# Kernel optimization log

Hardware: AMD Instinct MI355X
Metric: run time of the kernel (lower is better)

## Reference

```python
import jax, jax.numpy as jnp
import numpy as np
from jax import lax

DN = ('NCHW', 'OIHW', 'NCHW')

def conv7(x, w, b):
    y = lax.conv_general_dilated(x, w, window_strides=(1, 1), padding='VALID', dimension_numbers=DN)
    return y + b[None, :, None, None]

def maxpool2(x):
    return lax.reduce_window(x, -jnp.inf, lax.max, (1, 1, 2, 2), (1, 1, 2, 2), 'VALID')

def setup_inputs() -> dict:
    key = jax.random.key(0)
    ks = jax.random.split(key, 7)
    B, C, H, W = 8, 64, 70, 70
    x = jax.random.normal(ks[0], (B, C, H, W), dtype=jnp.float32)
    s = 0.05  # small init to keep softmax logits sane
    theta_w = jax.random.normal(ks[1], (100, C, 7, 7), dtype=jnp.float32) * s
    theta_b = jax.random.normal(ks[2], (100,), dtype=jnp.float32) * s
    phi_w = jax.random.normal(ks[3], (100, C, 7, 7), dtype=jnp.float32) * s
    phi_b = jax.random.normal(ks[4], (100,), dtype=jnp.float32) * s
    g_w = jax.random.normal(ks[5], (200, C, 7, 7), dtype=jnp.float32) * s
    g_b = jax.random.normal(ks[6], (200,), dtype=jnp.float32) * s
    return {'x': x, 'theta_w': theta_w, 'theta_b': theta_b, 'phi_w': phi_w, 'phi_b': phi_b, 'g_w': g_w, 'g_b': g_b}

def reference(x, theta_w, theta_b, phi_w, phi_b, g_w, g_b):
    B, C, H, W = x.shape
    h, w = H - 6, W - 6           # VALID 7x7 conv output spatial
    N = h * w                     # 4096
    M = N // 4                    # 1024 (after 2x2 maxpool)
    theta = conv7(x, theta_w, theta_b).reshape(B, 100, N)
    phi = maxpool2(conv7(x, phi_w, phi_b)).reshape(B, 100, M)
    attn = jnp.einsum('bcn,bcm->bnm', theta, phi)                # B x N x M
    attn = jax.nn.softmax(attn, axis=-1)
    g = maxpool2(conv7(x, g_w, g_b)).reshape(B, 200, M)
    attn_g = jnp.einsum('bcm,bnm->bcn', g, attn)
    return attn_g.reshape(B, 200, h, w)
```

## Files before the change

kernel.cpp:

```cpp
#include <hip/hip_runtime.h>
#include <cstdint>
#include <cstddef>

#define BATCH 8
#define CIN 64
#define HIN 70
#define HOUT 64
#define NPIX 4096
#define MPIX 1024

typedef __attribute__((ext_vector_type(8))) short short8;
typedef __attribute__((ext_vector_type(4))) float f32x4;
typedef __attribute__((ext_vector_type(4))) unsigned int uint4v;

__device__ __forceinline__ unsigned short f2bf_rne(float f) {
  unsigned int u = __builtin_bit_cast(unsigned int, f);
  unsigned int r = (u + 0x7FFFu + ((u >> 16) & 1u)) >> 16;
  return (unsigned short)r;
}

__device__ __forceinline__ unsigned int rot16(unsigned int u) {
  return (u >> 16) | (u << 16);
}

__global__ __launch_bounds__(256) void prep_x(const float* __restrict__ x,
                                              unsigned int* __restrict__ xTi,
                                              unsigned int* __restrict__ xTi_h) {
  __shared__ float tile[64][71];
  const int blk = blockIdx.x;
  const int b = blk / 70;
  const int r = blk - b * 70;
  const int t = threadIdx.x;
  for (int i = t; i < 64 * 70; i += 256) {
    int ci = i / 70;
    int c = i - ci * 70;
    tile[ci][c] = x[(((size_t)(b * 64 + ci)) * 70 + r) * 70 + c];
  }
  __syncthreads();
  for (int i = t; i < 70 * 64; i += 256) {
    int c = i >> 6;
    int ci = i & 63;
    float a = tile[ci][c];
    unsigned short hi = f2bf_rne(a);
    float hif = __builtin_bit_cast(float, ((unsigned int)hi) << 16);
    unsigned short lo = f2bf_rne(a - hif);
    xTi[(((size_t)(b * 70 + r)) * 70 + c) * 64 + ci] =
        (unsigned int)hi | (((unsigned int)lo) << 16);
  }
  for (int i = t; i < 70 * 32; i += 256) {
    int c = i >> 5;
    int dwi = i & 31;
    unsigned int h0 = f2bf_rne(tile[2 * dwi][c]);
    unsigned int h1 = f2bf_rne(tile[2 * dwi + 1][c]);
    xTi_h[(((size_t)(b * 70 + r)) * 70 + c) * 32 + dwi] = h0 | (h1 << 16);
  }
}

__global__ __launch_bounds__(256) void prep_w(
    const float* __restrict__ tw, const float* __restrict__ pw,
    const float* __restrict__ gw,
    const float* __restrict__ tb, const float* __restrict__ pb,
    const float* __restrict__ gb,
    unsigned int* __restrict__ wTi, unsigned int* __restrict__ wTi_s,
    float* __restrict__ biasPad) {
  int gid = blockIdx.x * 256 + threadIdx.x;
  if (gid < 1404928) {
    if (gid < 448) {
      float bv = 0.0f;
      if (gid < 100) bv = tb[gid];
      else if (gid < 200) bv = pb[gid - 100];
      else if (gid < 400) bv = gb[gid - 200];
      biasPad[gid] = bv;
    }
    int ci = gid & 63;
    int OC = (gid >> 6) % 448;
    int s = gid / (448 * 64);
    float v = 0.0f;
    if (OC < 100) v = tw[((size_t)(OC * 64 + ci)) * 49 + s];
    else if (OC < 200) v = pw[((size_t)((OC - 100) * 64 + ci)) * 49 + s];
    else if (OC < 400) v = gw[((size_t)((OC - 200) * 64 + ci)) * 49 + s];
    unsigned short hi = f2bf_rne(v);
    float hif = __builtin_bit_cast(float, ((unsigned int)hi) << 16);
    unsigned short lo = f2bf_rne(v - hif);
    wTi[gid] = (unsigned int)hi | (((unsigned int)lo) << 16);
  } else if (gid < 1404928 + 301056) {
    int g2 = gid - 1404928;
    int dwi = g2 & 31;
    int OCl = (g2 >> 5) % 192;
    int s = g2 / (192 * 32);
    int gc = 56 + OCl;
    float v0 = 0.0f, v1 = 0.0f;
    if (gc < 200) {
      v0 = gw[((size_t)(gc * 64 + 2 * dwi)) * 49 + s];
      v1 = gw[((size_t)(gc * 64 + 2 * dwi + 1)) * 49 + s];
    }
    wTi_s[g2] = (unsigned int)f2bf_rne(v0) |
                (((unsigned int)f2bf_rne(v1)) << 16);
  }
}

template <bool DUAL>
__global__ __launch_bounds__(256, 2) void convmfma_kernel(
    const unsigned short* __restrict__ xT,
    const unsigned short* __restrict__ wT,
    const float* __restrict__ biasPad,
    unsigned int* __restrict__ thd_dw,
    unsigned int* __restrict__ phd_dw,
    unsigned short* __restrict__ gP) {
  __shared__ __align__(16) char smem[62720 + 16384];
  const int LDSW = 62720;
  const int NCH = DUAL ? 4 : 2;
  const int XS = DUAL ? 128 : 64;
  const int WOCS = DUAL ? 128 : 64;
  const int WSTRIDE = DUAL ? 57344 : 12288;

  const int gx = blockIdx.x;
  const int b = gx >> 3;
  const int ptile = gx & 7;
  const int oy0 = ptile * 8;
  const int oc0 = (DUAL ? 0 : 256) + (blockIdx.y << 6);
  const int oc0W = DUAL ? oc0 : (blockIdx.y << 6);

  const int t = threadIdx.x;
  const int wv = t >> 6;
  const int l = t & 63;
  const int lm = l & 15;
  const int lg = l >> 4;

  int wdstOff_[2];
  const unsigned short* wsrc_[2];
  const int keyA = ((lm >> 1) & 3) << 4;
  const int laneA = (lm << 6) + ((lg << 4) ^ keyA);

  f32x4 acc[4][2][4];
#pragma unroll
  for (int j = 0; j < 4; ++j)
#pragma unroll
    for (int rr = 0; rr < 2; ++rr)
#pragma unroll
      for (int f = 0; f < 4; ++f) acc[j][rr][f] = (f32x4)0.0f;

  for (int chunk = 0; chunk < NCH; ++chunk) {
    for (int i = t; i < 3920; i += 256) {
      int idx70 = i >> 2;
      int s16 = i & 3;
      int rr = idx70 / 70;
      int cc = idx70 - rr * 70;
      const unsigned short* src =
          xT + ((size_t)((b * 70 + oy0 + rr) * 70 + cc)) * XS +
          (chunk << 5) + (s16 << 3);
      short8 v = *(const short8*)src;
      int dst = (idx70 << 6) + ((s16 << 4) ^ (((cc >> 1) & 3) << 4));
      *(short8*)(smem + dst) = v;
    }
    short8 wreg[2];
#pragma unroll
    for (int u2 = 0; u2 < 2; ++u2) {
      int u = t + (u2 << 8);
      int sub = u >> 8;
      int oc_t = (u >> 2) & 63;
      int q = u & 3;
      wdstOff_[u2] =
          sub * 4096 + (oc_t << 6) + ((q << 4) ^ (((oc_t >> 1) & 3) << 4));
      wsrc_[u2] = wT + (size_t)(oc0W + oc_t) * WOCS + (chunk << 5) + (q << 3);
      wreg[u2] = *(const short8*)(wsrc_[u2] + (size_t)sub * WSTRIDE);
      *(short8*)(smem + LDSW + wdstOff_[u2]) = wreg[u2];
      wreg[u2] = *(const short8*)(wsrc_[u2] + (size_t)(2 + sub) * WSTRIDE);
    }
    __syncthreads();

    for (int p = 0; p < 25; ++p) {
      const char* slotBase = smem + LDSW + ((p & 1) << 13);
#pragma unroll
      for (int halfs = 0; halfs < 2; ++halfs) {
        const int s = 2 * p + halfs;
        if (s <= 48) {
          const int ky = s / 7;
          const int kx = s - ky * 7;
          const char* wb = slotBase + (halfs << 12) + laneA;
          short8 aW[4], aS[4];
#pragma unroll
          for (int j = 0; j < 4; ++j) {
            aW[j] = *(const short8*)(wb + j * 1024);
            if (DUAL) {
              uint4v u = __builtin_bit_cast(uint4v, aW[j]);
              u.x = rot16(u.x); u.y = rot16(u.y);
              u.z = rot16(u.z); u.w = rot16(u.w);
              aS[j] = __builtin_bit_cast(short8, u);
            }
          }
          const int klx = kx + lm;
          const int key = ((klx >> 1) & 3) << 4;
#pragma unroll
          for (int rr = 0; rr < 2; ++rr) {
            const char* bbase =
                smem + ((2 * wv + rr + ky) * 70 + klx) * 64 + ((lg << 4) ^ key);
#pragma unroll
            for (int f = 0; f < 4; ++f) {
              short8 bf = *(const short8*)(bbase + f * 1024);
#pragma unroll
              for (int j = 0; j < 4; ++j) {
                acc[j][rr][f] = __builtin_amdgcn_mfma_f32_16x16x32_bf16(
                    aW[j], bf, acc[j][rr][f], 0, 0, 0);
                if (DUAL)
                  acc[j][rr][f] = __builtin_amdgcn_mfma_f32_16x16x32_bf16(
                      aS[j], bf, acc[j][rr][f], 0, 0, 0);
              }
            }
          }
        }
      }
      if (p < 24) {
#pragma unroll
        for (int u2 = 0; u2 < 2; ++u2) {
          *(short8*)(smem + LDSW + (((p + 1) & 1) << 13) + wdstOff_[u2]) =
              wreg[u2];
          if (p < 23) {
            int sub = (t + (u2 << 8)) >> 8;
            int snext = 2 * (p + 2) + sub;
            if (snext > 48) snext = 48;
            wreg[u2] = *(const short8*)(wsrc_[u2] + (size_t)snext * WSTRIDE);
          }
        }
      }
      __syncthreads();
    }
  }

  float bia[4][4];
#pragma unroll
  for (int j = 0; j < 4; ++j)
#pragma unroll
    for (int r = 0; r < 4; ++r) bia[j][r] = biasPad[oc0 + j * 16 + lg * 4 + r];

  if (DUAL) {
#pragma unroll
    for (int j = 0; j < 4; ++j) {
#pragma unroll
      for (int rr = 0; rr < 2; ++rr) {
#pragma unroll
        for (int f = 0; f < 4; ++f) {
#pragma unroll
          for (int r = 0; r < 4; ++r) {
            int ch = oc0 + j * 16 + lg * 4 + r;
            if (ch < 128) {
              int n = (oy0 + 2 * wv + rr) * 64 + f * 16 + lm;
              unsigned int outw = 0u;
              if (ch < 100) {
                float v = acc[j][rr][f][r] + bia[j][r];
                unsigned short hi = f2bf_rne(v);
                float hif =
                    __builtin_bit_cast(float, ((unsigned int)hi) << 16);
                unsigned short lo = f2bf_rne(v - hif);
                outw = (unsigned int)hi | (((unsigned int)lo) << 16);
              }
              thd_dw[(((size_t)(b << 12) + n) << 7) + ch] = outw;
            }
          }
        }
      }
    }
  }

#pragma unroll
  for (int j = 0; j < 4; ++j) {
#pragma unroll
    for (int f = 0; f < 4; ++f) {
#pragma unroll
      for (int r = 0; r < 4; ++r) {
        float v0 = acc[j][0][f][r] + bia[j][r];
        float v1 = acc[j][1][f][r] + bia[j][r];
        float vr = fmaxf(v0, v1);
        float vn = fmaxf(vr, __shfl_xor(vr, 1));
        if (!(lm & 1)) {
          int ch = oc0 + j * 16 + lg * 4 + r;
          int m = (((oy0 >> 1) + wv) << 5) + f * 8 + (lm >> 1);
          if (DUAL) {
            if (ch >= 100 && ch < 200) {
              int c = ch - 100;
              unsigned short hi = f2bf_rne(vn);
              float hif = __builtin_bit_cast(float, ((unsigned int)hi) << 16);
              unsigned short lo = f2bf_rne(vn - hif);
              phd_dw[(((size_t)(b << 10) + m) << 7) + c] =
                  (unsigned int)hi | (((unsigned int)lo) << 16);
            } else if (ch >= 200) {
              gP[((size_t)(b * 208 + (ch - 200)) << 10) + m] = f2bf_rne(vn);
              if (ch < 228)
                phd_dw[(((size_t)(b << 10) + m) << 7) + (ch - 100)] = 0u;
            }
          } else {
            int cg = ch - 200;
            if (cg < 208)
              gP[((size_t)(b * 208 + cg) << 10) + m] = f2bf_rne(vn);
          }
        }
      }
    }
  }
}

__global__ __launch_bounds__(256) void attn_kernel(
    const unsigned short* __restrict__ thd,
    const unsigned short* __restrict__ phd,
    const unsigned short* __restrict__ gP,
    float* __restrict__ out) {
  __shared__ __align__(16) float outAcc[16][212];
  __shared__ float corrL[16][33];
  __shared__ float statsL[4][16][2];
  __shared__ float mFinL[16];
  __shared__ float invL[16];

  const int bx = blockIdx.x;
  const int b = bx >> 8;
  const int n0 = (bx & 255) << 4;
  const int t = threadIdx.x;
  const int w = t >> 6;
  const int l = t & 63;
  const int lm = l & 15;
  const int lg = l >> 4;

  short8 aA[8], aS[8];
  {
    const unsigned short* ap =
        thd + (((size_t)(b << 12) + n0 + lm) << 8) + lg * 8;
#pragma unroll
    for (int kf = 0; kf < 8; ++kf) {
      short8 v = *(const short8*)(ap + kf * 32);
      aA[kf] = v;
      uint4v u = __builtin_bit_cast(uint4v, v);
      u.x = rot16(u.x); u.y = rot16(u.y); u.z = rot16(u.z); u.w = rot16(u.w);
      aS[kf] = __builtin_bit_cast(short8, u);
    }
  }

  float mRun = -3.0e38f, sRun = 0.0f;
  unsigned int Pr[8][4];

  const int src1 = ((lg & 1) << 5) + lm;
  const int src2 = src1 + 16;
  const bool hi2 = (lg >> 1) != 0;

#pragma unroll
  for (int step = 0; step < 8; ++step) {
    const int m0 = (w << 8) + (step << 5);
    f32x4 ac0 = (f32x4)0.f, ac1 = (f32x4)0.f;
    const unsigned short* bp0 =
        phd + (((size_t)(b << 10) + m0 + lm) << 8) + lg * 8;
    const unsigned short* bp1 = bp0 + (16 << 8);
#pragma unroll
    for (int kf = 0; kf < 8; ++kf) {
      short8 av0 = *(const short8*)(bp0 + kf * 32);
      short8 av1 = *(const short8*)(bp1 + kf * 32);
      ac0 = __builtin_amdgcn_mfma_f32_16x16x32_bf16(av0, aA[kf], ac0, 0, 0, 0);
      ac1 = __builtin_amdgcn_mfma_f32_16x16x32_bf16(av1, aA[kf], ac1, 0, 0, 0);
      ac0 = __builtin_amdgcn_mfma_f32_16x16x32_bf16(av0, aS[kf], ac0, 0, 0, 0);
      ac1 = __builtin_amdgcn_mfma_f32_16x16x32_bf16(av1, aS[kf], ac1, 0, 0, 0);
    }
    float tm = fmaxf(fmaxf(fmaxf(ac0[0], ac0[1]), fmaxf(ac0[2], ac0[3])),
                     fmaxf(fmaxf(ac1[0], ac1[1]), fmaxf(ac1[2], ac1[3])));
    tm = fmaxf(tm, __shfl_xor(tm, 16));
    tm = fmaxf(tm, __shfl_xor(tm, 32));
    float mNew = fmaxf(mRun, tm);
    float scale = __expf(mRun - mNew);
    float p0 = __expf(ac0[0] - mNew), p1 = __expf(ac0[1] - mNew);
    float p2 = __expf(ac0[2] - mNew), p3 = __expf(ac0[3] - mNew);
    float q0 = __expf(ac1[0] - mNew), q1 = __expf(ac1[1] - mNew);
    float q2 = __expf(ac1[2] - mNew), q3 = __expf(ac1[3] - mNew);
    float cs = ((p0 + p1) + (p2 + p3)) + ((q0 + q1) + (q2 + q3));
    cs += __shfl_xor(cs, 16);
    cs += __shfl_xor(cs, 32);
    mRun = mNew;
    sRun = sRun * scale + cs;
    if (l < 16) corrL[lm][(w << 3) + step] = mRun;
    unsigned int d0 = (unsigned int)f2bf_rne(p0) |
                      (((unsigned int)f2bf_rne(p1)) << 16);
    unsigned int d1 = (unsigned int)f2bf_rne(p2) |
                      (((unsigned int)f2bf_rne(p3)) << 16);
    unsigned int e0 = (unsigned int)f2bf_rne(q0) |
                      (((unsigned int)f2bf_rne(q1)) << 16);
    unsigned int e1 = (unsigned int)f2bf_rne(q2) |
                      (((unsigned int)f2bf_rne(q3)) << 16);
    unsigned int A0 = (unsigned int)__shfl((int)d0, src1);
    unsigned int A1 = (unsigned int)__shfl((int)d1, src1);
    unsigned int B0 = (unsigned int)__shfl((int)d0, src2);
    unsigned int B1 = (unsigned int)__shfl((int)d1, src2);
    unsigned int C0 = (unsigned int)__shfl((int)e0, src1);
    unsigned int C1 = (unsigned int)__shfl((int)e1, src1);
    unsigned int D0 = (unsigned int)__shfl((int)e0, src2);
    unsigned int D1 = (unsigned int)__shfl((int)e1, src2);
    Pr[step][0] = hi2 ? C0 : A0;
    Pr[step][1] = hi2 ? C1 : A1;
    Pr[step][2] = hi2 ? D0 : B0;
    Pr[step][3] = hi2 ? D1 : B1;
  }
  if (l < 16) {
    statsL[w][lm][0] = mRun;
    statsL[w][lm][1] = sRun;
  }
  __syncthreads();

  if (t < 16) {
    float mF = -3.0e38f;
#pragma unroll
    for (int qq = 0; qq < 4; ++qq) mF = fmaxf(mF, statsL[qq][t][0]);
    float sF = 0.0f;
#pragma unroll
    for (int qq = 0; qq < 4; ++qq)
      sF += statsL[qq][t][1] * __expf(statsL[qq][t][0] - mF);
    mFinL[t] = mF;
    invL[t] = 1.0f / sF;
  }
  __syncthreads();

  {
    int e = t * 2;
#pragma unroll
    for (int i = 0; i < 2; ++i) {
      int row = (e + i) >> 5;
      int col = (e + i) & 31;
      corrL[row][col] = __expf(corrL[row][col] - mFinL[row]) * invL[row];
    }
  }
  __syncthreads();

#pragma unroll
  for (int s = 0; s < 8; ++s) {
    float corr = corrL[lm][(w << 3) + s];
#pragma unroll
    for (int j = 0; j < 4; ++j) {
      unsigned int u = Pr[s][j];
      float lo = __builtin_bit_cast(float, u << 16);
      float hi = __builtin_bit_cast(float, u & 0xffff0000u);
      Pr[s][j] = (unsigned int)f2bf_rne(lo * corr) |
                 (((unsigned int)f2bf_rne(hi * corr)) << 16);
    }
  }

  f32x4 oacc[13];
#pragma unroll
  for (int i = 0; i < 13; ++i) oacc[i] = (f32x4)0.f;

#pragma unroll
  for (int s = 0; s < 8; ++s) {
    uint4v pu;
    pu.x = Pr[s][0]; pu.y = Pr[s][1]; pu.z = Pr[s][2]; pu.w = Pr[s][3];
    short8 pf = __builtin_bit_cast(short8, pu);
    const unsigned short* gbase =
        gP + ((size_t)(b * 208) << 10) + (w << 8) + (s << 5) + lg * 8;
#pragma unroll
    for (int ct = 0; ct < 13; ++ct) {
      int c = (ct << 4) + lm;
      short8 gv = *(const short8*)(gbase + ((size_t)c << 10));
      oacc[ct] = __builtin_amdgcn_mfma_f32_16x16x32_bf16(pf, gv, oacc[ct], 0, 0, 0);
    }
  }

  for (int rnd = 0; rnd < 4; ++rnd) {
    if (w == rnd) {
#pragma unroll
      for (int ct = 0; ct < 13; ++ct) {
#pragma unroll
        for (int r = 0; r < 4; ++r) {
          int n = (lg << 2) + r;
          int c = (ct << 4) + lm;
          if (rnd == 0) outAcc[n][c] = oacc[ct][r];
          else outAcc[n][c] += oacc[ct][r];
        }
      }
    }
    __syncthreads();
  }

  {
    int lane16 = t & 15;
    int grp = t >> 4;
    for (int c = grp; c < 200; c += 16)
      out[(((size_t)(b * 200 + c)) << 12) + n0 + lane16] = outAcc[lane16][c];
  }
}

extern "C" void kernel_launch(void* const* d_in, const int* in_sizes, int n_in,
                              void* d_out, int out_size, void* d_ws,
                              size_t ws_size, hipStream_t stream) {
  const float* x  = (const float*)d_in[0];
  const float* tw = (const float*)d_in[1];
  const float* tb = (const float*)d_in[2];
  const float* pw = (const float*)d_in[3];
  const float* pb = (const float*)d_in[4];
  const float* gw = (const float*)d_in[5];
  const float* gb = (const float*)d_in[6];
  float* out = (float*)d_out;

  unsigned short* ws_us = (unsigned short*)d_ws;
  unsigned short* thd   = ws_us;
  unsigned short* phd   = ws_us + 8388608;
  unsigned short* gP    = ws_us + 10485760;
  unsigned short* xTi   = ws_us + 12189696;
  unsigned short* wTi   = ws_us + 17207296;
  unsigned short* xTi_h = ws_us + 20017152;
  unsigned short* wTi_s = ws_us + 22525952;
  float* biasPad = (float*)(ws_us + 23128064);

  prep_x<<<560, 256, 0, stream>>>(x, (unsigned int*)xTi, (unsigned int*)xTi_h);
  prep_w<<<6664, 256, 0, stream>>>(tw, pw, gw, tb, pb, gb,
                                   (unsigned int*)wTi, (unsigned int*)wTi_s,
                                   biasPad);

  convmfma_kernel<true><<<dim3(64, 4), 256, 0, stream>>>(
      xTi, wTi, biasPad, (unsigned int*)thd, (unsigned int*)phd, gP);
  convmfma_kernel<false><<<dim3(64, 3), 256, 0, stream>>>(
      xTi_h, wTi_s, biasPad, (unsigned int*)thd, (unsigned int*)phd, gP);
  attn_kernel<<<2048, 256, 0, stream>>>(thd, phd, gP, out);
}
```

Before: 445.1 us.

## Process 32 query rows per attention block to reuse phi and g loads

The attention kernel now handles two 16-row query tiles per block instead of one, halving the grid. Each phi fragment loaded from global memory feeds MFMAs for both query tiles, and the softmax state, LDS buffers and output staging are widened to match. The g-side MFMA phase runs once per query half, and the cross-wave LDS reduction is staggered by column class so waves write in parallel rather than one at a time. Rot16 copies are now recomputed inside the loop to save registers. This raises register pressure and halves block count, which may lower occupancy.

```diff
diff --git a/kernel.cpp b/kernel.cpp
--- a/kernel.cpp
+++ b/kernel.cpp
@@ -21,6 +21,12 @@
 
 __device__ __forceinline__ unsigned int rot16(unsigned int u) {
   return (u >> 16) | (u << 16);
+}
+
+__device__ __forceinline__ short8 rot16x4(short8 v) {
+  uint4v u = __builtin_bit_cast(uint4v, v);
+  u.x = rot16(u.x); u.y = rot16(u.y); u.z = rot16(u.z); u.w = rot16(u.w);
+  return __builtin_bit_cast(short8, u);
 }
 
 __global__ __launch_bounds__(256) void prep_x(const float* __restrict__ x,
@@ -182,12 +188,7 @@
 #pragma unroll
           for (int j = 0; j < 4; ++j) {
             aW[j] = *(const short8*)(wb + j * 1024);
-            if (DUAL) {
-              uint4v u = __builtin_bit_cast(uint4v, aW[j]);
-              u.x = rot16(u.x); u.y = rot16(u.y);
-              u.z = rot16(u.z); u.w = rot16(u.w);
-              aS[j] = __builtin_bit_cast(short8, u);
-            }
+            if (DUAL) aS[j] = rot16x4(aW[j]);
           }
           const int klx = kx + lm;
           const int key = ((klx >> 1) & 3) << 4;
@@ -304,37 +305,36 @@
     const unsigned short* __restrict__ phd,
     const unsigned short* __restrict__ gP,
     float* __restrict__ out) {
-  __shared__ __align__(16) float outAcc[16][212];
-  __shared__ float corrL[16][33];
-  __shared__ float statsL[4][16][2];
-  __shared__ float mFinL[16];
-  __shared__ float invL[16];
+  __shared__ __align__(16) float outAcc[32][212];
+  __shared__ float corrL[32][33];
+  __shared__ float statsL[4][32][2];
+  __shared__ float mFinL[32];
+  __shared__ float invL[32];
 
   const int bx = blockIdx.x;
-  const int b = bx >> 8;
-  const int n0 = (bx & 255) << 4;
+  const int b = bx >> 7;
+  const int n0 = (bx & 127) << 5;
   const int t = threadIdx.x;
   const int w = t >> 6;
   const int l = t & 63;
   const int lm = l & 15;
   const int lg = l >> 4;
 
-  short8 aA[8], aS[8];
+  short8 aA0[8], aA1[8];
   {
-    const unsigned short* ap =
+    const unsigned short* ap0 =
         thd + (((size_t)(b << 12) + n0 + lm) << 8) + lg * 8;
+    const unsigned short* ap1 = ap0 + (16 << 8);
 #pragma unroll
     for (int kf = 0; kf < 8; ++kf) {
-      short8 v = *(const short8*)(ap + kf * 32);
-      aA[kf] = v;
-      uint4v u = __builtin_bit_cast(uint4v, v);
-      u.x = rot16(u.x); u.y = rot16(u.y); u.z = rot16(u.z); u.w = rot16(u.w);
-      aS[kf] = __builtin_bit_cast(short8, u);
-    }
-  }
-
-  float mRun = -3.0e38f, sRun = 0.0f;
-  unsigned int Pr[8][4];
+      aA0[kf] = *(const short8*)(ap0 + kf * 32);
+      aA1[kf] = *(const short8*)(ap1 + kf * 32);
+    }
+  }
+
+  float mRun0 = -3.0e38f, sRun0 = 0.0f;
+  float mRun1 = -3.0e38f, sRun1 = 0.0f;
+  unsigned int Pr0[8][4], Pr1[8][4];
 
   const int src1 = ((lg & 1) << 5) + lm;
   const int src2 = src1 + 16;
@@ -343,7 +343,8 @@
 #pragma unroll
   for (int step = 0; step < 8; ++step) {
     const int m0 = (w << 8) + (step << 5);
-    f32x4 ac0 = (f32x4)0.f, ac1 = (f32x4)0.f;
+    f32x4 a00 = (f32x4)0.f, a01 = (f32x4)0.f;
+    f32x4 a10 = (f32x4)0.f, a11 = (f32x4)0.f;
     const unsigned short* bp0 =
         phd + (((size_t)(b << 10) + m0 + lm) << 8) + lg * 8;
     const unsigned short* bp1 = bp0 + (16 << 8);
@@ -351,55 +352,103 @@
     for (int kf = 0; kf < 8; ++kf) {
       short8 av0 = *(const short8*)(bp0 + kf * 32);
       short8 av1 = *(const short8*)(bp1 + kf * 32);
-      ac0 = __builtin_amdgcn_mfma_f32_16x16x32_bf16(av0, aA[kf], ac0, 0, 0, 0);
-      ac1 = __builtin_amdgcn_mfma_f32_16x16x32_bf16(av1, aA[kf], ac1, 0, 0, 0);
-      ac0 = __builtin_amdgcn_mfma_f32_16x16x32_bf16(av0, aS[kf], ac0, 0, 0, 0);
-      ac1 = __builtin_amdgcn_mfma_f32_16x16x32_bf16(av1, aS[kf], ac1, 0, 0, 0);
-    }
-    float tm = fmaxf(fmaxf(fmaxf(ac0[0], ac0[1]), fmaxf(ac0[2], ac0[3])),
-                     fmaxf(fmaxf(ac1[0], ac1[1]), fmaxf(ac1[2], ac1[3])));
-    tm = fmaxf(tm, __shfl_xor(tm, 16));
-    tm = fmaxf(tm, __shfl_xor(tm, 32));
-    float mNew = fmaxf(mRun, tm);
-    float scale = __expf(mRun - mNew);
-    float p0 = __expf(ac0[0] - mNew), p1 = __expf(ac0[1] - mNew);
-    float p2 = __expf(ac0[2] - mNew), p3 = __expf(ac0[3] - mNew);
-    float q0 = __expf(ac1[0] - mNew), q1 = __expf(ac1[1] - mNew);
-    float q2 = __expf(ac1[2] - mNew), q3 = __expf(ac1[3] - mNew);
-    float cs = ((p0 + p1) + (p2 + p3)) + ((q0 + q1) + (q2 + q3));
-    cs += __shfl_xor(cs, 16);
-    cs += __shfl_xor(cs, 32);
-    mRun = mNew;
-    sRun = sRun * scale + cs;
-    if (l < 16) corrL[lm][(w << 3) + step] = mRun;
-    unsigned int d0 = (unsigned int)f2bf_rne(p0) |
-                      (((unsigned int)f2bf_rne(p1)) << 16);
-    unsigned int d1 = (unsigned int)f2bf_rne(p2) |
-                      (((unsigned int)f2bf_rne(p3)) << 16);
-    unsigned int e0 = (unsigned int)f2bf_rne(q0) |
-                      (((unsigned int)f2bf_rne(q1)) << 16);
-    unsigned int e1 = (unsigned int)f2bf_rne(q2) |
-                      (((unsigned int)f2bf_rne(q3)) << 16);
-    unsigned int A0 = (unsigned int)__shfl((int)d0, src1);
-    unsigned int A1 = (unsigned int)__shfl((int)d1, src1);
-    unsigned int B0 = (unsigned int)__shfl((int)d0, src2);
-    unsigned int B1 = (unsigned int)__shfl((int)d1, src2);
-    unsigned int C0 = (unsigned int)__shfl((int)e0, src1);
-    unsigned int C1 = (unsigned int)__shfl((int)e1, src1);
-    unsigned int D0 = (unsigned int)__shfl((int)e0, src2);
-    unsigned int D1 = (unsigned int)__shfl((int)e1, src2);
-    Pr[step][0] = hi2 ? C0 : A0;
-    Pr[step][1] = hi2 ? C1 : A1;
-    Pr[step][2] = hi2 ? D0 : B0;
-    Pr[step][3] = hi2 ? D1 : B1;
+      short8 s0 = rot16x4(aA0[kf]);
+      short8 s1 = rot16x4(aA1[kf]);
+      a00 = __builtin_amdgcn_mfma_f32_16x16x32_bf16(av0, aA0[kf], a00, 0, 0, 0);
+      a01 = __builtin_amdgcn_mfma_f32_16x16x32_bf16(av1, aA0[kf], a01, 0, 0, 0);
+      a00 = __builtin_amdgcn_mfma_f32_16x16x32_bf16(av0, s0, a00, 0, 0, 0);
+      a01 = __builtin_amdgcn_mfma_f32_16x16x32_bf16(av1, s0, a01, 0, 0, 0);
+      a10 = __builtin_amdgcn_mfma_f32_16x16x32_bf16(av0, aA1[kf], a10, 0, 0, 0);
+      a11 = __builtin_amdgcn_mfma_f32_16x16x32_bf16(av1, aA1[kf], a11, 0, 0, 0);
+      a10 = __builtin_amdgcn_mfma_f32_16x16x32_bf16(av0, s1, a10, 0, 0, 0);
+      a11 = __builtin_amdgcn_mfma_f32_16x16x32_bf16(av1, s1, a11, 0, 0, 0);
+    }
+    {
+      float tm = fmaxf(fmaxf(fmaxf(a00[0], a00[1]), fmaxf(a00[2], a00[3])),
+                       fmaxf(fmaxf(a01[0], a01[1]), fmaxf(a01[2], a01[3])));
+      tm = fmaxf(tm, __shfl_xor(tm, 16));
+      tm = fmaxf(tm, __shfl_xor(tm, 32));
+      float mNew = fmaxf(mRun0, tm);
+      float scale = __expf(mRun0 - mNew);
+      float p0 = __expf(a00[0] - mNew), p1 = __expf(a00[1] - mNew);
+      float p2 = __expf(a00[2] - mNew), p3 = __expf(a00[3] - mNew);
+      float q0 = __expf(a01[0] - mNew), q1 = __expf(a01[1] - mNew);
+      float q2 = __expf(a01[2] - mNew), q3 = __expf(a01[3] - mNew);
+      float cs = ((p0 + p1) + (p2 + p3)) + ((q0 + q1) + (q2 + q3));
+      cs += __shfl_xor(cs, 16);
+      cs += __shfl_xor(cs, 32);
+      mRun0 = mNew;
+      sRun0 = sRun0 * scale + cs;
+      if (l < 16) corrL[lm][(w << 3) + step] = mRun0;
+      unsigned int d0 = (unsigned int)f2bf_rne(p0) |
+                        (((unsigned int)f2bf_rne(p1)) << 16);
+      unsigned int d1 = (unsigned int)f2bf_rne(p2) |
+                        (((unsigned int)f2bf_rne(p3)) << 16);
+      unsigned int e0 = (unsigned int)f2bf_rne(q0) |
+                        (((unsigned int)f2bf_rne(q1)) << 16);
+      unsigned int e1 = (unsigned int)f2bf_rne(q2) |
+                        (((unsigned int)f2bf_rne(q3)) << 16);
+      unsigned int A0 = (unsigned int)__shfl((int)d0, src1);
+      unsigned int A1 = (unsigned int)__shfl((int)d1, src1);
+      unsigned int B0 = (unsigned int)__shfl((int)d0, src2);
+      unsigned int B1 = (unsigned int)__shfl((int)d1, src2);
+      unsigned int C0 = (unsigned int)__shfl((int)e0, src1);
+      unsigned int C1 = (unsigned int)__shfl((int)e1, src1);
+      unsigned int D0 = (unsigned int)__shfl((int)e0, src2);
+      unsigned int D1 = (unsigned int)__shfl((int)e1, src2);
+      Pr0[step][0] = hi2 ? C0 : A0;
+      Pr0[step][1] = hi2 ? C1 : A1;
+      Pr0[step][2] = hi2 ? D0 : B0;
+      Pr0[step][3] = hi2 ? D1 : B1;
+    }
+    {
+      float tm = fmaxf(fmaxf(fmaxf(a10[0], a10[1]), fmaxf(a10[2], a10[3])),
+                       fmaxf(fmaxf(a11[0], a11[1]), fmaxf(a11[2], a11[3])));
+      tm = fmaxf(tm, __shfl_xor(tm, 16));
+      tm = fmaxf(tm, __shfl_xor(tm, 32));
+      float mNew = fmaxf(mRun1, tm);
+      float scale = __expf(mRun1 - mNew);
+      float p0 = __expf(a10[0] - mNew), p1 = __expf(a10[1] - mNew);
+      float p2 = __expf(a10[2] - mNew), p3 = __expf(a10[3] - mNew);
+      float q0 = __expf(a11[0] - mNew), q1 = __expf(a11[1] - mNew);
+      float q2 = __expf(a11[2] - mNew), q3 = __expf(a11[3] - mNew);
+      float cs = ((p0 + p1) + (p2 + p3)) + ((q0 + q1) + (q2 + q3));
+      cs += __shfl_xor(cs, 16);
+      cs += __shfl_xor(cs, 32);
+      mRun1 = mNew;
+      sRun1 = sRun1 * scale + cs;
+      if (l < 16) corrL[lm + 16][(w << 3) + step] = mRun1;
+      unsigned int d0 = (unsigned int)f2bf_rne(p0) |
+                        (((unsigned int)f2bf_rne(p1)) << 16);
+      unsigned int d1 = (unsigned int)f2bf_rne(p2) |
+                        (((unsigned int)f2bf_rne(p3)) << 16);
+      unsigned int e0 = (unsigned int)f2bf_rne(q0) |
+                        (((unsigned int)f2bf_rne(q1)) << 16);
+      unsigned int e1 = (unsigned int)f2bf_rne(q2) |
+                        (((unsigned int)f2bf_rne(q3)) << 16);
+      unsigned int A0 = (unsigned int)__shfl((int)d0, src1);
+      unsigned int A1 = (unsigned int)__shfl((int)d1, src1);
+      unsigned int B0 = (unsigned int)__shfl((int)d0, src2);
+      unsigned int B1 = (unsigned int)__shfl((int)d1, src2);
+      unsigned int C0 = (unsigned int)__shfl((int)e0, src1);
+      unsigned int C1 = (unsigned int)__shfl((int)e1, src1);
+      unsigned int D0 = (unsigned int)__shfl((int)e0, src2);
+      unsigned int D1 = (unsigned int)__shfl((int)e1, src2);
+      Pr1[step][0] = hi2 ? C0 : A0;
+      Pr1[step][1] = hi2 ? C1 : A1;
+      Pr1[step][2] = hi2 ? D0 : B0;
+      Pr1[step][3] = hi2 ? D1 : B1;
+    }
   }
   if (l < 16) {
-    statsL[w][lm][0] = mRun;
-    statsL[w][lm][1] = sRun;
+    statsL[w][lm][0] = mRun0;
+    statsL[w][lm][1] = sRun0;
+    statsL[w][lm + 16][0] = mRun1;
+    statsL[w][lm + 16][1] = sRun1;
   }
   __syncthreads();
 
-  if (t < 16) {
+  if (t < 32) {
     float mF = -3.0e38f;
 #pragma unroll
     for (int qq = 0; qq < 4; ++qq) mF = fmaxf(mF, statsL[qq][t][0]);
@@ -413,11 +462,12 @@
   __syncthreads();
 
   {
-    int e = t * 2;
-#pragma unroll
-    for (int i = 0; i < 2; ++i) {
-      int row = (e + i) >> 5;
-      int col = (e + i) & 31;
+    int e = t * 4;
+#pragma unroll
+    for (int i = 0; i < 4; ++i) {
+      int idx = e + i;
+      int row = idx >> 5;
+      int col = idx & 31;
       corrL[row][col] = __expf(corrL[row][col] - mFinL[row]) * invL[row];
     }
   }
@@ -425,57 +475,73 @@
 
 #pragma unroll
   for (int s = 0; s < 8; ++s) {
-    float corr = corrL[lm][(w << 3) + s];
+    float c0 = corrL[lm][(w << 3) + s];
+    float c1 = corrL[lm + 16][(w << 3) + s];
 #pragma unroll
     for (int j = 0; j < 4; ++j) {
-      unsigned int u = Pr[s][j];
-      float lo = __builtin_bit_cast(float, u << 16);
-      float hi = __builtin_bit_cast(float, u & 0xffff0000u);
-      Pr[s][j] = (unsigned int)f2bf_rne(lo * corr) |
-                 (((unsigned int)f2bf_rne(hi * corr)) << 16);
-    }
-  }
-
-  f32x4 oacc[13];
-#pragma unroll
-  for (int i = 0; i < 13; ++i) oacc[i] = (f32x4)0.f;
-
-#pragma unroll
-  for (int s = 0; s < 8; ++s) {
-    uint4v pu;
-    pu.x = Pr[s][0]; pu.y = Pr[s][1]; pu.z = Pr[s][2]; pu.w = Pr[s][3];
-    short8 pf = __builtin_bit_cast(short8, pu);
-    const unsigned short* gbase =
-        gP + ((size_t)(b * 208) << 10) + (w << 8) + (s << 5) + lg * 8;
-#pragma unroll
-    for (int ct = 0; ct < 13; ++ct) {
-      int c = (ct << 4) + lm;
-      short8 gv = *(const short8*)(gbase + ((size_t)c << 10));
-      oacc[ct] = __builtin_amdgcn_mfma_f32_16x16x32_bf16(pf, gv, oacc[ct], 0, 0, 0);
-    }
-  }
-
-  for (int rnd = 0; rnd < 4; ++rnd) {
-    if (w == rnd) {
-#pragma unroll
-      for (int ct = 0; ct < 13; ++ct) {
-#pragma unroll
-        for (int r = 0; r < 4; ++r) {
-          int n = (lg << 2) + r;
-          int c = (ct << 4) + lm;
-          if (rnd == 0) outAcc[n][c] = oacc[ct][r];
-          else outAcc[n][c] += oacc[ct][r];
-        }
+      {
+        unsigned int u = Pr0[s][j];
+        float lo = __builtin_bit_cast(float, u << 16);
+        float hi = __builtin_bit_cast(float, u & 0xffff0000u);
+        Pr0[s][j] = (unsigned int)f2bf_rne(lo * c0) |
+                    (((unsigned int)f2bf_rne(hi * c0)) << 16);
       }
-    }
-    __syncthreads();
-  }
+      {
+        unsigned int u = Pr1[s][j];
+        float lo = __builtin_bit_cast(float, u << 16);
+        float hi = __builtin_bit_cast(float, u & 0xffff0000u);
+        Pr1[s][j] = (unsigned int)f2bf_rne(lo * c1) |
+                    (((unsigned int)f2bf_rne(hi * c1)) << 16);
+      }
+    }
+  }
+
+#define PHASE_C(PRX, NH)                                                      \
+  {                                                                           \
+    f32x4 oacc[13];                                                           \
+    _Pragma("unroll") for (int i = 0; i < 13; ++i) oacc[i] = (f32x4)0.f;      \
+    _Pragma("unroll") for (int s = 0; s < 8; ++s) {                           \
+      uint4v pu;                                                              \
+      pu.x = PRX[s][0]; pu.y = PRX[s][1];                                     \
+      pu.z = PRX[s][2]; pu.w = PRX[s][3];                                     \
+      short8 pf = __builtin_bit_cast(short8, pu);                             \
+      const unsigned short* gbase =                                           \
+          gP + ((size_t)(b * 208) << 10) + (w << 8) + (s << 5) + lg * 8;      \
+      _Pragma("unroll") for (int ct = 0; ct < 13; ++ct) {                     \
+        int c = (ct << 4) + lm;                                               \
+        short8 gv = *(const short8*)(gbase + ((size_t)c << 10));              \
+        oacc[ct] =                                                            \
+            __builtin_amdgcn_mfma_f32_16x16x32_bf16(pf, gv, oacc[ct], 0, 0, 0); \
+      }                                                                       \
+    }                                                                         \
+    for (int rnd = 0; rnd < 4; ++rnd) {                                       \
+      const int cls = (w + rnd) & 3;                                          \
+      _Pragma("unroll") for (int ct = 0; ct < 13; ++ct) {                     \
+        if ((ct & 3) == cls) {                                                \
+          _Pragma("unroll") for (int r = 0; r < 4; ++r) {                     \
+            int n = (NH << 4) + (lg << 2) + r;                                \
+            int c = (ct << 4) + lm;                                           \
+            if (rnd == 0) outAcc[n][c] = oacc[ct][r];                         \
+            else outAcc[n][c] += oacc[ct][r];                                 \
+          }                                                                   \
+        }                                                                     \
+      }                                                                       \
+      __syncthreads();                                                        \
+    }                                                                         \
+  }
+
+  PHASE_C(Pr0, 0)
+  PHASE_C(Pr1, 1)
+#undef PHASE_C
 
   {
     int lane16 = t & 15;
     int grp = t >> 4;
-    for (int c = grp; c < 200; c += 16)
-      out[(((size_t)(b * 200 + c)) << 12) + n0 + lane16] = outAcc[lane16][c];
+    for (int c = grp; c < 200; c += 16) {
+      float* op = out + (((size_t)(b * 200 + c)) << 12) + n0 + lane16;
+      op[0] = outAcc[lane16][c];
+      op[16] = outAcc[16 + lane16][c];
+    }
   }
 }
 
@@ -510,5 +576,5 @@
       xTi, wTi, biasPad, (unsigned int*)thd, (unsigned int*)phd, gP);
   convmfma_kernel<false><<<dim3(64, 3), 256, 0, stream>>>(
       xTi_h, wTi_s, biasPad, (unsigned int*)thd, (unsigned int*)phd, gP);
-  attn_kernel<<<2048, 256, 0, stream>>>(thd, phd, gP, out);
-}
+  attn_kernel<<<1024, 256, 0, stream>>>(thd, phd, gP, out);
+}
```

Result: slower. 487.3 us (+9.5%).

## Fuse PV accumulation into online softmax loop with running rescale

Applied to the files above, without the earlier changes.

The attention kernel now accumulates P·G inside the per-step softmax loop, FlashAttention style. The output accumulators are rescaled only when the running max changes, detected with a wave-wide vote. This drops the stored per-step P registers, the corrL shared array and its pass, and the post-hoc bf16 re-rounding of P. The rotated theta copies are also recomputed per use instead of held in registers, which lowers register pressure but adds occasional accumulator rescales and interleaves G loads with the QK MFMAs.

```diff
diff --git a/kernel.cpp b/kernel.cpp
--- a/kernel.cpp
+++ b/kernel.cpp
@@ -21,6 +21,12 @@
 
 __device__ __forceinline__ unsigned int rot16(unsigned int u) {
   return (u >> 16) | (u << 16);
+}
+
+__device__ __forceinline__ short8 rot16x4(short8 v) {
+  uint4v u = __builtin_bit_cast(uint4v, v);
+  u.x = rot16(u.x); u.y = rot16(u.y); u.z = rot16(u.z); u.w = rot16(u.w);
+  return __builtin_bit_cast(short8, u);
 }
 
 __global__ __launch_bounds__(256) void prep_x(const float* __restrict__ x,
@@ -182,12 +188,7 @@
 #pragma unroll
           for (int j = 0; j < 4; ++j) {
             aW[j] = *(const short8*)(wb + j * 1024);
-            if (DUAL) {
-              uint4v u = __builtin_bit_cast(uint4v, aW[j]);
-              u.x = rot16(u.x); u.y = rot16(u.y);
-              u.z = rot16(u.z); u.w = rot16(u.w);
-              aS[j] = __builtin_bit_cast(short8, u);
-            }
+            if (DUAL) aS[j] = rot16x4(aW[j]);
           }
           const int klx = kx + lm;
           const int key = ((klx >> 1) & 3) << 4;
@@ -305,7 +306,6 @@
     const unsigned short* __restrict__ gP,
     float* __restrict__ out) {
   __shared__ __align__(16) float outAcc[16][212];
-  __shared__ float corrL[16][33];
   __shared__ float statsL[4][16][2];
   __shared__ float mFinL[16];
   __shared__ float invL[16];
@@ -319,26 +319,23 @@
   const int lm = l & 15;
   const int lg = l >> 4;
 
-  short8 aA[8], aS[8];
+  short8 aA[8];
   {
     const unsigned short* ap =
         thd + (((size_t)(b << 12) + n0 + lm) << 8) + lg * 8;
 #pragma unroll
-    for (int kf = 0; kf < 8; ++kf) {
-      short8 v = *(const short8*)(ap + kf * 32);
-      aA[kf] = v;
-      uint4v u = __builtin_bit_cast(uint4v, v);
-      u.x = rot16(u.x); u.y = rot16(u.y); u.z = rot16(u.z); u.w = rot16(u.w);
-      aS[kf] = __builtin_bit_cast(short8, u);
-    }
+    for (int kf = 0; kf < 8; ++kf) aA[kf] = *(const short8*)(ap + kf * 32);
   }
 
   float mRun = -3.0e38f, sRun = 0.0f;
-  unsigned int Pr[8][4];
+  f32x4 oacc[13];
+#pragma unroll
+  for (int i = 0; i < 13; ++i) oacc[i] = (f32x4)0.f;
 
   const int src1 = ((lg & 1) << 5) + lm;
   const int src2 = src1 + 16;
   const bool hi2 = (lg >> 1) != 0;
+  const int rbase = lg << 2;
 
 #pragma unroll
   for (int step = 0; step < 8; ++step) {
@@ -351,17 +348,19 @@
     for (int kf = 0; kf < 8; ++kf) {
       short8 av0 = *(const short8*)(bp0 + kf * 32);
       short8 av1 = *(const short8*)(bp1 + kf * 32);
+      short8 sw = rot16x4(aA[kf]);
       ac0 = __builtin_amdgcn_mfma_f32_16x16x32_bf16(av0, aA[kf], ac0, 0, 0, 0);
       ac1 = __builtin_amdgcn_mfma_f32_16x16x32_bf16(av1, aA[kf], ac1, 0, 0, 0);
-      ac0 = __builtin_amdgcn_mfma_f32_16x16x32_bf16(av0, aS[kf], ac0, 0, 0, 0);
-      ac1 = __builtin_amdgcn_mfma_f32_16x16x32_bf16(av1, aS[kf], ac1, 0, 0, 0);
-    }
+      ac0 = __builtin_amdgcn_mfma_f32_16x16x32_bf16(av0, sw, ac0, 0, 0, 0);
+      ac1 = __builtin_amdgcn_mfma_f32_16x16x32_bf16(av1, sw, ac1, 0, 0, 0);
+    }
+    const float mOld = mRun;
     float tm = fmaxf(fmaxf(fmaxf(ac0[0], ac0[1]), fmaxf(ac0[2], ac0[3])),
                      fmaxf(fmaxf(ac1[0], ac1[1]), fmaxf(ac1[2], ac1[3])));
     tm = fmaxf(tm, __shfl_xor(tm, 16));
     tm = fmaxf(tm, __shfl_xor(tm, 32));
-    float mNew = fmaxf(mRun, tm);
-    float scale = __expf(mRun - mNew);
+    const float mNew = fmaxf(mOld, tm);
+    const float scale = __expf(mOld - mNew);
     float p0 = __expf(ac0[0] - mNew), p1 = __expf(ac0[1] - mNew);
     float p2 = __expf(ac0[2] - mNew), p3 = __expf(ac0[3] - mNew);
     float q0 = __expf(ac1[0] - mNew), q1 = __expf(ac1[1] - mNew);
@@ -369,9 +368,8 @@
     float cs = ((p0 + p1) + (p2 + p3)) + ((q0 + q1) + (q2 + q3));
     cs += __shfl_xor(cs, 16);
     cs += __shfl_xor(cs, 32);
+    sRun = sRun * scale + cs;
     mRun = mNew;
-    sRun = sRun * scale + cs;
-    if (l < 16) corrL[lm][(w << 3) + step] = mRun;
     unsigned int d0 = (unsigned int)f2bf_rne(p0) |
                       (((unsigned int)f2bf_rne(p1)) << 16);
     unsigned int d1 = (unsigned int)f2bf_rne(p2) |
@@ -388,11 +386,35 @@
     unsigned int C1 = (unsigned int)__shfl((int)e1, src1);
     unsigned int D0 = (unsigned int)__shfl((int)e0, src2);
     unsigned int D1 = (unsigned int)__shfl((int)e1, src2);
-    Pr[step][0] = hi2 ? C0 : A0;
-    Pr[step][1] = hi2 ? C1 : A1;
-    Pr[step][2] = hi2 ? D0 : B0;
-    Pr[step][3] = hi2 ? D1 : B1;
-  }
+    uint4v pu;
+    pu.x = hi2 ? C0 : A0;
+    pu.y = hi2 ? C1 : A1;
+    pu.z = hi2 ? D0 : B0;
+    pu.w = hi2 ? D1 : B1;
+    short8 pf = __builtin_bit_cast(short8, pu);
+    if (!__all(mNew == mOld)) {
+      float s0 = __shfl(scale, rbase + 0);
+      float s1 = __shfl(scale, rbase + 1);
+      float s2 = __shfl(scale, rbase + 2);
+      float s3 = __shfl(scale, rbase + 3);
+#pragma unroll
+      for (int ct = 0; ct < 13; ++ct) {
+        oacc[ct][0] *= s0;
+        oacc[ct][1] *= s1;
+        oacc[ct][2] *= s2;
+        oacc[ct][3] *= s3;
+      }
+    }
+    const unsigned short* gbase =
+        gP + ((size_t)(b * 208) << 10) + m0 + lg * 8;
+#pragma unroll
+    for (int ct = 0; ct < 13; ++ct) {
+      int c = (ct << 4) + lm;
+      short8 gv = *(const short8*)(gbase + ((size_t)c << 10));
+      oacc[ct] = __builtin_amdgcn_mfma_f32_16x16x32_bf16(pf, gv, oacc[ct], 0, 0, 0);
+    }
+  }
+
   if (l < 16) {
     statsL[w][lm][0] = mRun;
     statsL[w][lm][1] = sRun;
@@ -413,45 +435,17 @@
   __syncthreads();
 
   {
-    int e = t * 2;
-#pragma unroll
-    for (int i = 0; i < 2; ++i) {
-      int row = (e + i) >> 5;
-      int col = (e + i) & 31;
-      corrL[row][col] = __expf(corrL[row][col] - mFinL[row]) * invL[row];
-    }
-  }
-  __syncthreads();
-
-#pragma unroll
-  for (int s = 0; s < 8; ++s) {
-    float corr = corrL[lm][(w << 3) + s];
-#pragma unroll
-    for (int j = 0; j < 4; ++j) {
-      unsigned int u = Pr[s][j];
-      float lo = __builtin_bit_cast(float, u << 16);
-      float hi = __builtin_bit_cast(float, u & 0xffff0000u);
-      Pr[s][j] = (unsigned int)f2bf_rne(lo * corr) |
-                 (((unsigned int)f2bf_rne(hi * corr)) << 16);
-    }
-  }
-
-  f32x4 oacc[13];
-#pragma unroll
-  for (int i = 0; i < 13; ++i) oacc[i] = (f32x4)0.f;
-
-#pragma unroll
-  for (int s = 0; s < 8; ++s) {
-    uint4v pu;
-    pu.x = Pr[s][0]; pu.y = Pr[s][1]; pu.z = Pr[s][2]; pu.w = Pr[s][3];
-    short8 pf = __builtin_bit_cast(short8, pu);
-    const unsigned short* gbase =
-        gP + ((size_t)(b * 208) << 10) + (w << 8) + (s << 5) + lg * 8;
+    float corrMe = __expf(mRun - mFinL[lm]) * invL[lm];
+    float c0 = __shfl(corrMe, rbase + 0);
+    float c1 = __shfl(corrMe, rbase + 1);
+    float c2 = __shfl(corrMe, rbase + 2);
+    float c3 = __shfl(corrMe, rbase + 3);
 #pragma unroll
     for (int ct = 0; ct < 13; ++ct) {
-      int c = (ct << 4) + lm;
-      short8 gv = *(const short8*)(gbase + ((size_t)c << 10));
-      oacc[ct] = __builtin_amdgcn_mfma_f32_16x16x32_bf16(pf, gv, oacc[ct], 0, 0, 0);
+      oacc[ct][0] *= c0;
+      oacc[ct][1] *= c1;
+      oacc[ct][2] *= c2;
+      oacc[ct][3] *= c3;
     }
   }
 
@@ -461,7 +455,7 @@
       for (int ct = 0; ct < 13; ++ct) {
 #pragma unroll
         for (int r = 0; r < 4; ++r) {
-          int n = (lg << 2) + r;
+          int n = rbase + r;
           int c = (ct << 4) + lm;
           if (rnd == 0) outAcc[n][c] = oacc[ct][r];
           else outAcc[n][c] += oacc[ct][r];
```

After: 476.0 us. 1.07x slower.
